# Performance work log

Measured on AMD Instinct MI355X. Metric: run time of the kernel, lower is better.

## Reference

```python
import jax, jax.numpy as jnp
import numpy as np

B, M, KM, D, H, L = 8, 2048, 1024, 256, 4, 2
HD = D // H

def _sp(x):
    return jnp.logaddexp(x, 0.0)  # softplus

def _rot_half(x):
    s = x.shape
    x = x.reshape(s[:-1] + (s[-1] // 2, 2))
    return jnp.stack((-x[..., 1], x[..., 0]), -1).reshape(s)

def _posenc(Wr, xy):
    # LearnableFourierPositionalEncoding(2, head_dim): rotary cos/sin embedding
    proj = xy @ Wr.T                                     # [N, HD//2]
    emb = jnp.stack((jnp.cos(proj), jnp.sin(proj)), 0)   # [2, N, HD//2]
    return jnp.repeat(emb, 2, axis=-1)                   # [2, N, HD]

def _heads(t):
    return t.reshape(t.shape[0], H, HD).transpose(1, 0, 2)  # [H, N, HD]

def _unheads(t):
    return t.transpose(1, 0, 2).reshape(t.shape[1], D)

def _ffn(x, m, W1, b1, g, be, W2, b2):
    h = jnp.concatenate([x, m], -1) @ W1.T + b1
    mu = h.mean(-1, keepdims=True)
    v = ((h - mu) ** 2).mean(-1, keepdims=True)
    h = (h - mu) * jax.lax.rsqrt(v + 1e-5) * g + be
    return x + jax.nn.gelu(h, approximate=False) @ W2.T + b2

def _self_block(x, enc, Wqkv, bqkv, Wo, bo, W1, b1, g, be, W2, b2):
    N = x.shape[0]
    qkv = (x @ Wqkv.T + bqkv).reshape(N, H, HD, 3).transpose(1, 0, 2, 3)  # [H,N,HD,3]
    q, k, v = qkv[..., 0], qkv[..., 1], qkv[..., 2]
    q = q * enc[0] + _rot_half(q) * enc[1]
    k = k * enc[0] + _rot_half(k) * enc[1]
    attn = jax.nn.softmax(jnp.einsum('hid,hjd->hij', q, k) / jnp.sqrt(jnp.float32(HD)), -1)
    msg = _unheads(jnp.einsum('hij,hjd->hid', attn, v)) @ Wo.T + bo
    return _ffn(x, msg, W1, b1, g, be, W2, b2)

def _cross_block(x0, x1, Wqk, bqk, Wv, bv, Wo, bo, W1, b1, g, be, W2, b2):
    sc = HD ** -0.25
    qk0 = _heads(x0 @ Wqk.T + bqk) * sc
    qk1 = _heads(x1 @ Wqk.T + bqk) * sc
    v0 = _heads(x0 @ Wv.T + bv)
    v1 = _heads(x1 @ Wv.T + bv)
    sim = jnp.einsum('hid,hjd->hij', qk0, qk1)
    m0 = _unheads(jnp.einsum('hij,hjd->hid', jax.nn.softmax(sim, -1), v1)) @ Wo.T + bo
    m1 = _unheads(jnp.einsum('hij,hid->hjd', jax.nn.softmax(sim, -2), v0)) @ Wo.T + bo
    return _ffn(x0, m0, W1, b1, g, be, W2, b2), _ffn(x1, m1, W1, b1, g, be, W2, b2)

def _forward(features_a, features_b, matches, kpts_a, kpts_b, lam, beta, Wr,
             pW1, pb1, pW2, pb2,
             sWqkv, sbqkv, sWo, sbo, sW1, sb1, sg, sbe, sW2, sb2,
             cWqk, cbqk, cWv, cbv, cWo, cbo, cW1, cb1, cg, cbe, cW2, cb2):
    lam_r = _sp(lam) + 1e-6
    beta_r = _sp(beta)
    eye = jnp.eye(KM, dtype=jnp.float32)

    def per_sample(fa, fb, match, ka, kb):
        ia, ib = match[:, 0], match[:, 1]
        f_i = fb[ib] - fa[ia]                                   # [KM, D]
        xy0, xy1 = ka[ia, :2], kb[ib, :2]                       # [KM, 2]
        d2 = jnp.sum((xy0[:, None, :] - xy0[None, :, :]) ** 2, -1)
        Kmat = jnp.exp(-beta_r * d2)                            # Gaussian RKHS kernel
        Lc = jnp.linalg.cholesky(Kmat + lam_r * eye)
        C = jax.scipy.linalg.cho_solve((Lc, True), f_i)         # [KM, D]
        f_glob = (Kmat / (Kmat.sum(-1, keepdims=True) + 1e-6)) @ C
        enc0, enc1 = _posenc(Wr, xy0), _posenc(Wr, xy1)
        d0, d1 = f_i, f_glob
        for l in range(L):
            d0 = _self_block(d0, enc0, sWqkv[l], sbqkv[l], sWo[l], sbo[l], sW1[l], sb1[l], sg[l], sbe[l], sW2[l], sb2[l])
            d1 = _self_block(d1, enc1, sWqkv[l], sbqkv[l], sWo[l], sbo[l], sW1[l], sb1[l], sg[l], sbe[l], sW2[l], sb2[l])
            d0, d1 = _cross_block(d0, d1, cWqk[l], cbqk[l], cWv[l], cbv[l], cWo[l], cbo[l], cW1[l], cb1[l], cg[l], cbe[l], cW2[l], cb2[l])
        h = jax.nn.relu(d0 @ pW1.T + pb1)
        return jax.nn.sigmoid(h @ pW2.T + pb2)[:, 0]            # [KM]

    return jax.vmap(per_sample)(features_a, features_b, matches, kpts_a, kpts_b)

def setup_inputs() -> dict:
    key = jax.random.key(0)
    ks = iter(jax.random.split(key, 64))
    def n(shape, s=0.02):
        return jax.random.normal(next(ks), shape, jnp.float32) * s
    return {
        'features_a': n((B, M, D), 1.0),
        'features_b': n((B, M, D), 1.0),
        'matches': jax.random.randint(next(ks), (B, KM, 2), 0, M),
        'kpts_a': jax.random.uniform(next(ks), (B, M, 2), jnp.float32) * 32.0,
        'kpts_b': jax.random.uniform(next(ks), (B, M, 2), jnp.float32) * 32.0,
        'lam': jnp.float32(0.1),
        'beta': jnp.float32(1.0),
        'Wr': n((HD // 2, 2), 1.0),
        'pW1': n((64, D)), 'pb1': jnp.zeros((64,), jnp.float32),
        'pW2': n((1, 64)), 'pb2': jnp.zeros((1,), jnp.float32),
        'sWqkv': n((L, 3 * D, D)), 'sbqkv': jnp.zeros((L, 3 * D), jnp.float32),
        'sWo': n((L, D, D)), 'sbo': jnp.zeros((L, D), jnp.float32),
        'sW1': n((L, 2 * D, 2 * D)), 'sb1': jnp.zeros((L, 2 * D), jnp.float32),
        'sg': jnp.ones((L, 2 * D), jnp.float32), 'sbe': jnp.zeros((L, 2 * D), jnp.float32),
        'sW2': n((L, D, 2 * D)), 'sb2': jnp.zeros((L, D), jnp.float32),
        'cWqk': n((L, D, D)), 'cbqk': jnp.zeros((L, D), jnp.float32),
        'cWv': n((L, D, D)), 'cbv': jnp.zeros((L, D), jnp.float32),
        'cWo': n((L, D, D)), 'cbo': jnp.zeros((L, D), jnp.float32),
        'cW1': n((L, 2 * D, 2 * D)), 'cb1': jnp.zeros((L, 2 * D), jnp.float32),
        'cg': jnp.ones((L, 2 * D), jnp.float32), 'cbe': jnp.zeros((L, 2 * D), jnp.float32),
        'cW2': n((L, D, 2 * D)), 'cb2': jnp.zeros((L, D), jnp.float32),
    }

def reference(features_a, features_b, matches, kpts_a, kpts_b, lam, beta, Wr,
              pW1, pb1, pW2, pb2,
              sWqkv, sbqkv, sWo, sbo, sW1, sb1, sg, sbe, sW2, sb2,
              cWqk, cbqk, cWv, cbv, cWo, cbo, cW1, cb1, cg, cbe, cW2, cb2):
    return _forward(features_a, features_b, matches, kpts_a, kpts_b, lam, beta, Wr,
                    pW1, pb1, pW2, pb2,
                    sWqkv, sbqkv, sWo, sbo, sW1, sb1, sg, sbe, sW2, sb2,
                    cWqk, cbqk, cWv, cbv, cWo, cbo, cW1, cb1, cg, cbe, cW2, cb2)
```

## Files before the change

kernel.cpp:

```cpp
#include <hip/hip_runtime.h>
#include <math.h>

#define BB 8
#define MM 2048
#define KM 1024
#define DD 256
#define HH 4
#define HD 64
#define NLAYER 2
#define BN (BB*KM)
#define N2 (2*BN)
#define CG_ITERS 5

#define SWZ(r,c) (((r)<<6) + ((((c)>>3) ^ ((r)&7))<<3) + ((c)&7))

typedef __bf16 bf16;
typedef __bf16 bf16x8 __attribute__((ext_vector_type(8)));
typedef __bf16 bf16x4 __attribute__((ext_vector_type(4)));
typedef __bf16 bf16x2 __attribute__((ext_vector_type(2)));
typedef _Float16 fp16;
typedef _Float16 fp16x8 __attribute__((ext_vector_type(8)));
typedef short  short4v __attribute__((ext_vector_type(4)));
typedef float  floatx4 __attribute__((ext_vector_type(4)));
#define MFMA16(a,b,c)  __builtin_amdgcn_mfma_f32_16x16x32_bf16(a,b,c,0,0,0)
#define MFMA16H(a,b,c) __builtin_amdgcn_mfma_f32_16x16x32_f16(a,b,c,0,0,0)

#if defined(__HIP_DEVICE_COMPILE__)
  #if __has_builtin(__builtin_amdgcn_mfma_f32_16x16x16bf16_1k)
    #define MFMA1K(a,b,c) __builtin_amdgcn_mfma_f32_16x16x16bf16_1k(a,b,c,0,0,0)
  #else
    #error "device pass lacks mfma_f32_16x16x16bf16_1k"
  #endif
#else
  #define MFMA1K(a,b,c) (c)
#endif

__device__ __forceinline__ float softplusf(float x) {
  return fmaxf(x, 0.f) + log1pf(expf(-fabsf(x)));
}

__device__ __forceinline__ float wred(float x) {
  x += __shfl_xor(x, 1);  x += __shfl_xor(x, 2);  x += __shfl_xor(x, 4);
  x += __shfl_xor(x, 8);  x += __shfl_xor(x, 16); x += __shfl_xor(x, 32);
  return x;
}

__device__ __forceinline__ short4v pack4(float a, float b, float c, float d) {
  bf16x4 v = {(bf16)a,(bf16)b,(bf16)c,(bf16)d};
  short4v s;
  __builtin_memcpy(&s, &v, 8);
  return s;
}

__device__ __forceinline__ void stage8(bf16* dst, const float* src) {
  float4 a = *(const float4*)src;
  float4 b = *(const float4*)(src + 4);
  bf16x8 v = { (bf16)a.x,(bf16)a.y,(bf16)a.z,(bf16)a.w,
               (bf16)b.x,(bf16)b.y,(bf16)b.z,(bf16)b.w };
  *(bf16x8*)dst = v;
}
__device__ __forceinline__ void stage8(bf16* dst, const bf16* src) {
  *(uint4*)dst = *(const uint4*)src;
}

template<typename T> struct Raw8;
template<> struct Raw8<float> {
  float4 a, b;
  __device__ __forceinline__ void load(const float* s) {
    a = *(const float4*)s; b = *(const float4*)(s + 4);
  }
  __device__ __forceinline__ void store(fp16* d) const {
    fp16x8 v = { (fp16)a.x,(fp16)a.y,(fp16)a.z,(fp16)a.w,
                 (fp16)b.x,(fp16)b.y,(fp16)b.z,(fp16)b.w };
    *(fp16x8*)d = v;
  }
  __device__ __forceinline__ void storeb(bf16* d) const {
    bf16x8 v = { (bf16)a.x,(bf16)a.y,(bf16)a.z,(bf16)a.w,
                 (bf16)b.x,(bf16)b.y,(bf16)b.z,(bf16)b.w };
    *(bf16x8*)d = v;
  }
};
template<> struct Raw8<fp16> {
  uint4 u;
  __device__ __forceinline__ void load(const fp16* s) { u = *(const uint4*)s; }
  __device__ __forceinline__ void store(fp16* d) const { *(uint4*)d = u; }
};

__global__ __launch_bounds__(256) void gather_kernel(
    const float* __restrict__ fa, const float* __restrict__ fb,
    const int* __restrict__ matches, const float* __restrict__ ka,
    const float* __restrict__ kb, float* __restrict__ F,
    float* __restrict__ Fd,
    float* __restrict__ xy0, float* __restrict__ xy1)
{
  int si = blockIdx.x;
  int s  = si >> 10;
  int t  = threadIdx.x;
  int ia = matches[(size_t)si*2+0];
  int ib = matches[(size_t)si*2+1];
  float v = fb[((size_t)s*MM + ib)*DD + t] - fa[((size_t)s*MM + ia)*DD + t];
  F[(size_t)si*DD + t]  = v;
  Fd[(size_t)si*DD + t] = v;
  if (t == 0) {
    xy0[(size_t)si*2+0] = ka[((size_t)s*MM + ia)*2+0];
    xy0[(size_t)si*2+1] = ka[((size_t)s*MM + ia)*2+1];
    xy1[(size_t)si*2+0] = kb[((size_t)s*MM + ib)*2+0];
    xy1[(size_t)si*2+1] = kb[((size_t)s*MM + ib)*2+1];
  }
}

__global__ __launch_bounds__(256) void posenc_kernel(
    const float* __restrict__ xy, const float* __restrict__ Wr,
    float* __restrict__ enc)
{
  int t = threadIdx.x;
  int si = blockIdx.x*4 + (t >> 6);
  int s = si >> 10, i = si & 1023;
  int d = t & 63; int p = d >> 1;
  float x = xy[(size_t)si*2], y = xy[(size_t)si*2+1];
  float pr = Wr[p*2]*x + Wr[p*2+1]*y;
  enc[(((size_t)s*2+0)*KM + i)*HD + d] = cosf(pr);
  enc[(((size_t)s*2+1)*KM + i)*HD + d] = sinf(pr);
}

__global__ __launch_bounds__(256) void kmat_kernel(
    const float* __restrict__ xy0, const float* __restrict__ beta_ptr,
    fp16* __restrict__ Km, float* __restrict__ rowsum)
{
  __shared__ float redw[4];
  int si = blockIdx.x; int s = si >> 10;
  int t = threadIdx.x;
  int lane = t & 63, w = t >> 6;
  float beta_l2 = softplusf(beta_ptr[0]) * 1.442695040888963f;
  float xi = xy0[(size_t)si*2], yi = xy0[(size_t)si*2+1];
  const float* xys = xy0 + (size_t)s*KM*2;
  float sum = 0.f;
  for (int jj = 0; jj < 4; ++jj) {
    int j = jj*256 + t;
    float dx = xi - xys[j*2], dy = yi - xys[j*2+1];
    float v = exp2f(-beta_l2*(dx*dx + dy*dy));
    Km[(size_t)si*KM + j] = (fp16)v;
    sum += v;
  }
  sum = wred(sum);
  if (lane == 0) redw[w] = sum;
  __syncthreads();
  if (t == 0)
    rowsum[si] = ((redw[0]+redw[1]) + (redw[2]+redw[3])) + 1e-6f;
}

template<int NT, int WPERM, int DUALW,
         typename TA1, typename TA2, typename TW, typename TO>
__global__ __launch_bounds__(256) void mm_kernel(
    const TA1* __restrict__ A1, const TA2* __restrict__ A2, int K1, int K,
    const TW* __restrict__ W, const float* __restrict__ bias,
    const TW* __restrict__ Wb, const float* __restrict__ biasb,
    TO* __restrict__ C, int O, float scale, float scaleb,
    const float* __restrict__ resid)
{
  __shared__ __align__(16) bf16 Al[128*72];
  __shared__ __align__(16) bf16 Wl[NT*72];
  constexpr int MB = (NT == 128) ? 4 : 2;
  constexpr int WP = NT/32;
  int tid = threadIdx.x;
  int row0 = blockIdx.x*128, col0 = blockIdx.y*NT;
  int lane = tid & 63, w = tid >> 6;
  int wr = (NT == 128) ? (w>>1)*64 : w*32;
  int wc = (NT == 128) ? (w&1)*64 : 0;
  int lm = lane & 15, lq = lane >> 4;
  int srow = tid >> 3, sc8 = (tid & 7)*8;

  const TA1* aptr1[4]; const TA2* aptr2[4];
#pragma unroll
  for (int p = 0; p < 4; ++p) {
    int row = p*32 + srow;
    aptr1[p] = A1 + (size_t)(row0+row)*K1 + sc8;
    aptr2[p] = A2 + (size_t)(row0+row)*(K-K1) + sc8;
  }
  const TW* wptr[WP];
#pragma unroll
  for (int p = 0; p < WP; ++p) {
    int wg = col0 + p*32 + srow;
    const TW* wsrc; int wrow;
    if (DUALW && wg >= 256) { wsrc = Wb; wrow = wg - 256; }
    else { wsrc = W; wrow = WPERM ? ((wg & 255)*3 + (wg >> 8)) : wg; }
    wptr[p] = wsrc + (size_t)wrow*K + sc8;
  }

  floatx4 acc[MB][4];
#pragma unroll
  for (int mb = 0; mb < MB; ++mb)
#pragma unroll
    for (int nb = 0; nb < 4; ++nb) acc[mb][nb] = (floatx4){0.f,0.f,0.f,0.f};
  for (int k0 = 0; k0 < K; k0 += 64) {
    bool use1 = (k0 < K1);
#pragma unroll
    for (int p = 0; p < 4; ++p) {
      bf16* d = &Al[(p*32+srow)*72 + sc8];
      if (use1) stage8(d, aptr1[p] + k0);
      else      stage8(d, aptr2[p] + (k0 - K1));
    }
#pragma unroll
    for (int p = 0; p < WP; ++p)
      stage8(&Wl[(p*32+srow)*72 + sc8], wptr[p] + k0);
    __syncthreads();
    bf16x8 af[MB][2], bfr[4][2];
#pragma unroll
    for (int mb = 0; mb < MB; ++mb) {
      af[mb][0] = *(bf16x8*)&Al[(wr + mb*16 + lm)*72 + lq*8];
      af[mb][1] = *(bf16x8*)&Al[(wr + mb*16 + lm)*72 + 32 + lq*8];
    }
#pragma unroll
    for (int nb = 0; nb < 4; ++nb) {
      bfr[nb][0] = *(bf16x8*)&Wl[(wc + nb*16 + lm)*72 + lq*8];
      bfr[nb][1] = *(bf16x8*)&Wl[(wc + nb*16 + lm)*72 + 32 + lq*8];
    }
    __builtin_amdgcn_s_setprio(1);
#pragma unroll
    for (int mb = 0; mb < MB; ++mb)
#pragma unroll
      for (int nb = 0; nb < 4; ++nb) {
        acc[mb][nb] = MFMA16(af[mb][0], bfr[nb][0], acc[mb][nb]);
        acc[mb][nb] = MFMA16(af[mb][1], bfr[nb][1], acc[mb][nb]);
      }
    __builtin_amdgcn_s_setprio(0);
    __syncthreads();
  }
#pragma unroll
  for (int mb = 0; mb < MB; ++mb) {
#pragma unroll
    for (int nb = 0; nb < 4; ++nb) {
#pragma unroll
      for (int r = 0; r < 4; ++r) {
        int grow = row0 + wr + mb*16 + lq*4 + r;
        int gcol = col0 + wc + nb*16 + lm;
        float v = acc[mb][nb][r];
        float bv = 0.f, scl = scale;
        if (DUALW && gcol >= 256) {
          if (biasb) bv = biasb[gcol - 256];
          scl = scaleb;
        } else if (bias) {
          bv = bias[WPERM ? ((gcol & 255)*3 + (gcol >> 8)) : gcol];
        }
        v = (v + bv) * scl;
        if (resid) v += resid[(size_t)grow*O + gcol];
        C[(size_t)grow*O + gcol] = (TO)v;
      }
    }
  }
}

template<typename TO>
__global__ __launch_bounds__(256) void mm64d_kernel(
    const bf16* __restrict__ A, int K, const float* __restrict__ W,
    const float* __restrict__ bias, TO* __restrict__ C, int O,
    const float* __restrict__ resid)
{
  __shared__ __align__(16) bf16 Al[2][64*72];
  __shared__ __align__(16) bf16 Wl[2][64*72];
  int tid = threadIdx.x;
  int row0 = blockIdx.x*64, col0 = blockIdx.y*64;
  int lane = tid & 63, w = tid >> 6;
  int wr = (w>>1)*32, wc = (w&1)*32;
  int lm = lane & 15, lq = lane >> 4;
  int sr0 = tid >> 3, c8 = (tid & 7)*8;
  int sr1 = sr0 + 32;
  const bf16*  a0ptr = A + (size_t)(row0+sr0)*K + c8;
  const bf16*  a1ptr = A + (size_t)(row0+sr1)*K + c8;
  const float* w0ptr = W + (size_t)(col0+sr0)*K + c8;
  const float* w1ptr = W + (size_t)(col0+sr1)*K + c8;

  floatx4 acc[2][2];
#pragma unroll
  for (int mb = 0; mb < 2; ++mb)
#pragma unroll
    for (int nb = 0; nb < 2; ++nb) acc[mb][nb] = (floatx4){0.f,0.f,0.f,0.f};

  uint4 ra0 = *(const uint4*)a0ptr;
  uint4 ra1 = *(const uint4*)a1ptr;
  Raw8<float> rw0, rw1;
  rw0.load(w0ptr); rw1.load(w1ptr);
  *(uint4*)&Al[0][sr0*72 + c8] = ra0;
  *(uint4*)&Al[0][sr1*72 + c8] = ra1;
  rw0.storeb(&Wl[0][sr0*72 + c8]);
  rw1.storeb(&Wl[0][sr1*72 + c8]);
  __syncthreads();

  for (int k0 = 0; k0 < K; k0 += 64) {
    int cur = (k0 >> 6) & 1;
    bool pre = (k0 + 64 < K);
    if (pre) {
      ra0 = *(const uint4*)(a0ptr + k0 + 64);
      ra1 = *(const uint4*)(a1ptr + k0 + 64);
      rw0.load(w0ptr + k0 + 64);
      rw1.load(w1ptr + k0 + 64);
    }
    bf16x8 af0[2], af1[2], b0[2], b1[2];
#pragma unroll
    for (int mb = 0; mb < 2; ++mb) {
      af0[mb] = *(bf16x8*)&Al[cur][(wr + mb*16 + lm)*72 + lq*8];
      af1[mb] = *(bf16x8*)&Al[cur][(wr + mb*16 + lm)*72 + 32 + lq*8];
    }
#pragma unroll
    for (int nb = 0; nb < 2; ++nb) {
      b0[nb] = *(bf16x8*)&Wl[cur][(wc + nb*16 + lm)*72 + lq*8];
      b1[nb] = *(bf16x8*)&Wl[cur][(wc + nb*16 + lm)*72 + 32 + lq*8];
    }
    __builtin_amdgcn_s_setprio(1);
#pragma unroll
    for (int mb = 0; mb < 2; ++mb)
#pragma unroll
      for (int nb = 0; nb < 2; ++nb) {
        acc[mb][nb] = MFMA16(af0[mb], b0[nb], acc[mb][nb]);
        acc[mb][nb] = MFMA16(af1[mb], b1[nb], acc[mb][nb]);
      }
    __builtin_amdgcn_s_setprio(0);
    if (pre) {
      *(uint4*)&Al[cur^1][sr0*72 + c8] = ra0;
      *(uint4*)&Al[cur^1][sr1*72 + c8] = ra1;
      rw0.storeb(&Wl[cur^1][sr0*72 + c8]);
      rw1.storeb(&Wl[cur^1][sr1*72 + c8]);
    }
    __syncthreads();
  }
#pragma unroll
  for (int mb = 0; mb < 2; ++mb) {
#pragma unroll
    for (int nb = 0; nb < 2; ++nb) {
#pragma unroll
      for (int r = 0; r < 4; ++r) {
        int grow = row0 + wr + mb*16 + lq*4 + r;
        int gcol = col0 + wc + nb*16 + lm;
        float v = acc[mb][nb][r] + bias[gcol];
        if (resid) v += resid[(size_t)grow*O + gcol];
        C[(size_t)grow*O + gcol] = (TO)v;
      }
    }
  }
}

template<typename TA, typename TW, typename TO>
__global__ __launch_bounds__(256) void mv64_kernel(
    const TA* __restrict__ A, int K, const TW* __restrict__ W,
    TO* __restrict__ C, int O,
    const float* __restrict__ resid, const float* __restrict__ lam_ptr,
    const float* __restrict__ rowdiv,
    long zsA, long zsW, long zsC, long zsR)
{
  __shared__ __align__(16) fp16 Al[2][64*72];
  __shared__ __align__(16) fp16 Wl[2][64*72];
  int tid = threadIdx.x;
  int z = blockIdx.z;
  const TA* Az = A + (size_t)z*zsA;
  const TW* Wz = W + (size_t)z*zsW;
  TO* Cz = C + (size_t)z*zsC;
  const float* Rz = resid ? (resid + (size_t)z*zsR) : (const float*)0;
  int row0 = blockIdx.x*64, col0 = blockIdx.y*64;
  int lane = tid & 63, w = tid >> 6;
  int wr = (w>>1)*32, wc = (w&1)*32;
  int lm = lane & 15, lq = lane >> 4;
  int sr0 = tid >> 3, c8 = (tid & 7)*8;
  int sr1 = sr0 + 32;
  floatx4 acc[2][2];
#pragma unroll
  for (int mb = 0; mb < 2; ++mb)
#pragma unroll
    for (int nb = 0; nb < 2; ++nb) acc[mb][nb] = (floatx4){0.f,0.f,0.f,0.f};

  Raw8<TA> a0p, a1p; Raw8<TW> w0p, w1p;
  a0p.load(&Az[(size_t)(row0+sr0)*K + c8]);
  a1p.load(&Az[(size_t)(row0+sr1)*K + c8]);
  w0p.load(&Wz[(size_t)(col0+sr0)*K + c8]);
  w1p.load(&Wz[(size_t)(col0+sr1)*K + c8]);
  a0p.store(&Al[0][sr0*72 + c8]); a1p.store(&Al[0][sr1*72 + c8]);
  w0p.store(&Wl[0][sr0*72 + c8]); w1p.store(&Wl[0][sr1*72 + c8]);
  __syncthreads();

  for (int k0 = 0; k0 < K; k0 += 64) {
    int cur = (k0 >> 6) & 1;
    bool pre = (k0 + 64 < K);
    if (pre) {
      a0p.load(&Az[(size_t)(row0+sr0)*K + k0+64 + c8]);
      a1p.load(&Az[(size_t)(row0+sr1)*K + k0+64 + c8]);
      w0p.load(&Wz[(size_t)(col0+sr0)*K + k0+64 + c8]);
      w1p.load(&Wz[(size_t)(col0+sr1)*K + k0+64 + c8]);
    }
    fp16x8 a0[2], a1[2], b0[2], b1[2];
#pragma unroll
    for (int mb = 0; mb < 2; ++mb) {
      a0[mb] = *(fp16x8*)&Al[cur][(wr + mb*16 + lm)*72 + lq*8];
      a1[mb] = *(fp16x8*)&Al[cur][(wr + mb*16 + lm)*72 + 32 + lq*8];
    }
#pragma unroll
    for (int nb = 0; nb < 2; ++nb) {
      b0[nb] = *(fp16x8*)&Wl[cur][(wc + nb*16 + lm)*72 + lq*8];
      b1[nb] = *(fp16x8*)&Wl[cur][(wc + nb*16 + lm)*72 + 32 + lq*8];
    }
    __builtin_amdgcn_s_setprio(1);
#pragma unroll
    for (int mb = 0; mb < 2; ++mb)
#pragma unroll
      for (int nb = 0; nb < 2; ++nb) {
        acc[mb][nb] = MFMA16H(a0[mb], b0[nb], acc[mb][nb]);
        acc[mb][nb] = MFMA16H(a1[mb], b1[nb], acc[mb][nb]);
      }
    __builtin_amdgcn_s_setprio(0);
    if (pre) {
      a0p.store(&Al[cur^1][sr0*72 + c8]); a1p.store(&Al[cur^1][sr1*72 + c8]);
      w0p.store(&Wl[cur^1][sr0*72 + c8]); w1p.store(&Wl[cur^1][sr1*72 + c8]);
    }
    __syncthreads();
  }
  float lamv = 1.f;
  if (lam_ptr) lamv = softplusf(lam_ptr[0]) + 1e-6f;
#pragma unroll
  for (int mb = 0; mb < 2; ++mb) {
#pragma unroll
    for (int nb = 0; nb < 2; ++nb) {
#pragma unroll
      for (int r = 0; r < 4; ++r) {
        int grow = row0 + wr + mb*16 + lq*4 + r;
        int gcol = col0 + wc + nb*16 + lm;
        float v = acc[mb][nb][r];
        if (rowdiv) v /= rowdiv[(size_t)z*KM + grow];
        if (Rz) v += lamv * Rz[(size_t)grow*O + gcol];
        Cz[(size_t)grow*O + gcol] = (TO)v;
      }
    }
  }
}

__global__ __launch_bounds__(256) void gemm_f32_kernel(
    const float* __restrict__ A, int K,
    const float* __restrict__ W, const float* __restrict__ bias,
    float* __restrict__ C, int O)
{
  __shared__ float As[32][68];
  __shared__ float Ws[32][68];
  int t = threadIdx.x;
  int row0 = blockIdx.x * 64;
  int col0 = blockIdx.y * 64;
  int ti = t & 15, tj = t >> 4;
  float acc[4][4] = {};
  for (int k0 = 0; k0 < K; k0 += 32) {
#pragma unroll
    for (int p = 0; p < 2; ++p) {
      int idx = p*256 + t;
      int ar = idx >> 3, af = (idx & 7)*4;
      float4 av = *(const float4*)&A[(size_t)(row0+ar)*K + k0 + af];
      As[af+0][ar] = av.x; As[af+1][ar] = av.y;
      As[af+2][ar] = av.z; As[af+3][ar] = av.w;
      float4 wv = *(const float4*)&W[(size_t)(col0+ar)*K + k0 + af];
      Ws[af+0][ar] = wv.x; Ws[af+1][ar] = wv.y;
      Ws[af+2][ar] = wv.z; Ws[af+3][ar] = wv.w;
    }
    __syncthreads();
#pragma unroll
    for (int kk = 0; kk < 32; ++kk) {
      float4 a4 = *(float4*)&As[kk][ti*4];
      float4 b4 = *(float4*)&Ws[kk][tj*4];
      float a[4] = {a4.x, a4.y, a4.z, a4.w};
      float b[4] = {b4.x, b4.y, b4.z, b4.w};
#pragma unroll
      for (int x = 0; x < 4; ++x)
#pragma unroll
        for (int y = 0; y < 4; ++y) acc[x][y] += a[x]*b[y];
    }
    __syncthreads();
  }
#pragma unroll
  for (int x = 0; x < 4; ++x) {
    int r = row0 + ti*4 + x;
#pragma unroll
    for (int y = 0; y < 4; ++y) {
      int c = col0 + tj*4 + y;
      float v = fmaxf(acc[x][y] + bias[c], 0.f);
      C[(size_t)r*O + c] = v;
    }
  }
}

__global__ __launch_bounds__(256) void tinit_kernel(
    const float* __restrict__ F, float* __restrict__ PT, float* __restrict__ RT,
    float* __restrict__ XT)
{
  __shared__ float Ls[64][68];
  int t = threadIdx.x;
  int k0 = blockIdx.x*64, n0 = blockIdx.y*64, z = blockIdx.z;
#pragma unroll
  for (int p = 0; p < 4; ++p) {
    int idx = p*256 + t;
    int kr = idx >> 4, c4 = (idx & 15)*4;
    *(float4*)&Ls[kr][c4] = *(const float4*)&F[((size_t)z*KM + k0+kr)*DD + n0 + c4];
  }
  __syncthreads();
#pragma unroll
  for (int p = 0; p < 4; ++p) {
    int idx = p*256 + t;
    int nl = idx >> 4, k4 = (idx & 15)*4;
    float4 v = { Ls[k4+0][nl], Ls[k4+1][nl], Ls[k4+2][nl], Ls[k4+3][nl] };
    size_t o = ((size_t)z*DD + n0+nl)*KM + k0 + k4;
    *(float4*)&PT[o] = v;
    *(float4*)&RT[o] = v;
    float4 zr = {0.f,0.f,0.f,0.f};
    *(float4*)&XT[o] = zr;
  }
}

__global__ __launch_bounds__(256) void cg_update_kernel(
    float* __restrict__ XT, float* __restrict__ RT,
    float* __restrict__ PT, const float* __restrict__ APT)
{
  __shared__ float redw[12];
  int row = blockIdx.x;
  int t = threadIdx.x;
  int lane = t & 63, w = t >> 6;
  size_t base = (size_t)row*KM + (size_t)t*4;
  float4 p4 = *(float4*)&PT[base];
  float4 a4 = *(const float4*)&APT[base];
  float4 r4 = *(float4*)&RT[base];
  float4 x4 = *(float4*)&XT[base];
  float prr  = (r4.x*r4.x + r4.y*r4.y) + (r4.z*r4.z + r4.w*r4.w);
  float ppap = (p4.x*a4.x + p4.y*a4.y) + (p4.z*a4.z + p4.w*a4.w);
  prr = wred(prr); ppap = wred(ppap);
  if (lane == 0) { redw[w] = prr; redw[4+w] = ppap; }
  __syncthreads();
  float rr  = (redw[0]+redw[1]) + (redw[2]+redw[3]);
  float pap = (redw[4]+redw[5]) + (redw[6]+redw[7]);
  float alpha = (pap > 1e-30f) ? rr/pap : 0.f;
  x4.x += alpha*p4.x; x4.y += alpha*p4.y; x4.z += alpha*p4.z; x4.w += alpha*p4.w;
  r4.x -= alpha*a4.x; r4.y -= alpha*a4.y; r4.z -= alpha*a4.z; r4.w -= alpha*a4.w;
  *(float4*)&XT[base] = x4;
  *(float4*)&RT[base] = r4;
  float s = (r4.x*r4.x + r4.y*r4.y) + (r4.z*r4.z + r4.w*r4.w);
  s = wred(s);
  if (lane == 0) redw[8+w] = s;
  __syncthreads();
  float rrnew = (redw[8]+redw[9]) + (redw[10]+redw[11]);
  float beta = (rr > 1e-30f) ? rrnew/rr : 0.f;
  p4.x = r4.x + beta*p4.x; p4.y = r4.y + beta*p4.y;
  p4.z = r4.z + beta*p4.z; p4.w = r4.w + beta*p4.w;
  *(float4*)&PT[base] = p4;
}

__global__ __launch_bounds__(256) void rope_split_kernel(
    const bf16* __restrict__ qkv, const float* __restrict__ enc0,
    const float* __restrict__ enc1, bf16* __restrict__ Qo,
    bf16* __restrict__ Ko)
{
  int t = threadIdx.x;
  int r = blockIdx.x*2 + (t >> 7);
  int c = (t & 127)*2;
  int ts = r >> 10, i = r & 1023;
  int d = c & 63;
  const float* enc = (ts < BB) ? enc0 : enc1;
  int s = (ts < BB) ? ts : ts - BB;
  const float* eb = enc + (((size_t)s*2)*KM + i)*HD;
  float2 cs = *(const float2*)&eb[d];
  float2 sn = *(const float2*)&eb[(size_t)KM*HD + d];
  size_t base = (size_t)r*768;
  bf16x2 qv = *(const bf16x2*)&qkv[base + c];
  bf16x2 kv = *(const bf16x2*)&qkv[base + 256 + c];
  float q0 = (float)qv[0], q1 = (float)qv[1];
  float k0 = (float)kv[0], k1 = (float)kv[1];
  float oq0 = q0*cs.x - q1*sn.x, oq1 = q1*cs.y + q0*sn.y;
  float ok0 = k0*cs.x - k1*sn.x, ok1 = k1*cs.y + k0*sn.y;
  size_t o = (size_t)r*DD + c;
  bf16x2 qo = {(bf16)(0.1803368801f*oq0), (bf16)(0.1803368801f*oq1)};
  bf16x2 ko = {(bf16)ok0, (bf16)ok1};
  *(bf16x2*)&Qo[o] = qo;
  *(bf16x2*)&Ko[o] = ko;
}

__global__ __launch_bounds__(256) void vt_kernel(
    const bf16* __restrict__ Vin, int vstride, bf16* __restrict__ VT)
{
  __shared__ __align__(16) bf16 Ls[64*72];
  int tid = threadIdx.x;
  int zh = blockIdx.x;
  int ts = zh >> 2, h = zh & 3;
  int k0 = blockIdx.y * 64;
#pragma unroll
  for (int p = 0; p < 2; ++p) {
    int idx = p*256 + tid;
    int kr = idx >> 3, c8 = (idx & 7)*8;
    *(uint4*)&Ls[kr*72 + c8] =
      *(const uint4*)&Vin[((size_t)ts*KM + k0 + kr)*vstride + h*HD + c8];
  }
  __syncthreads();
#pragma unroll
  for (int p = 0; p < 2; ++p) {
    int idx = p*256 + tid;
    int dr = idx >> 3, k8 = (idx & 7)*8;
    bf16 tmp[8] __attribute__((aligned(16)));
#pragma unroll
    for (int j = 0; j < 8; ++j) tmp[j] = Ls[(k8+j)*72 + dr];
    *(uint4*)&VT[((size_t)zh*HD + dr)*KM + k0 + k8] = *(uint4*)tmp;
  }
}

__device__ __forceinline__ void mha_body(
    const bf16* __restrict__ Qg, const bf16* __restrict__ Kg,
    const bf16* __restrict__ VTg, bf16* __restrict__ Og,
    size_t qkbase, size_t obase, size_t vbase, int qkstride,
    int q0, int tid, bf16* Qs, bf16* Ks, bf16* Vt)
{
  int lane = tid & 63, w = tid >> 6;
  int lm = lane & 15, lq = lane >> 4;
  int r0 = tid >> 3, c8 = (tid & 7)*8;
  int r1 = r0 + 32;
  *(uint4*)&Qs[SWZ(r0,c8)] = *(const uint4*)&Qg[qkbase + (size_t)(q0+r0)*qkstride + c8];
  *(uint4*)&Qs[SWZ(r1,c8)] = *(const uint4*)&Qg[qkbase + (size_t)(q0+r1)*qkstride + c8];
  __syncthreads();
  bf16x8 qa0 = *(bf16x8*)&Qs[SWZ(w*16 + lm, lq*8)];
  bf16x8 qa1 = *(bf16x8*)&Qs[SWZ(w*16 + lm, 32 + lq*8)];
  short4v ones4;
  { bf16x4 o1 = {(bf16)1.f,(bf16)1.f,(bf16)1.f,(bf16)1.f};
    __builtin_memcpy(&ones4, &o1, 8); }
  float m_ = 0.f;
  floatx4 lacc = (floatx4){0.f,0.f,0.f,0.f};
  floatx4 oacc[4];
#pragma unroll
  for (int db = 0; db < 4; ++db) oacc[db] = (floatx4){0.f,0.f,0.f,0.f};

  for (int kt = 0; kt < KM; kt += 64) {
    __syncthreads();
    *(uint4*)&Ks[SWZ(r0,c8)] = *(const uint4*)&Kg[qkbase + (size_t)(kt+r0)*qkstride + c8];
    *(uint4*)&Ks[SWZ(r1,c8)] = *(const uint4*)&Kg[qkbase + (size_t)(kt+r1)*qkstride + c8];
    *(uint4*)&Vt[SWZ(r0,c8)] = *(const uint4*)&VTg[vbase + (size_t)r0*KM + kt + c8];
    *(uint4*)&Vt[SWZ(r1,c8)] = *(const uint4*)&VTg[vbase + (size_t)r1*KM + kt + c8];
    __syncthreads();
    floatx4 st[4];
    float negm = -m_;
    __builtin_amdgcn_s_setprio(1);
#pragma unroll
    for (int kb = 0; kb < 4; ++kb) {
      bf16x8 a0 = *(bf16x8*)&Ks[SWZ(kb*16 + lm, lq*8)];
      bf16x8 a1 = *(bf16x8*)&Ks[SWZ(kb*16 + lm, 32 + lq*8)];
      floatx4 acc = (floatx4){negm, negm, negm, negm};
      acc = MFMA16(a0, qa0, acc);
      acc = MFMA16(a1, qa1, acc);
      st[kb] = acc;
    }
    __builtin_amdgcn_s_setprio(0);
    float ma = fmaxf(fmaxf(st[0][0], st[0][1]), st[0][2]);
    float mb = fmaxf(fmaxf(st[0][3], st[1][0]), st[1][1]);
    float mc = fmaxf(fmaxf(st[1][2], st[1][3]), st[2][0]);
    float md = fmaxf(fmaxf(st[2][1], st[2][2]), st[2][3]);
    float me = fmaxf(fmaxf(st[3][0], st[3][1]), st[3][2]);
    float mf = fmaxf(fmaxf(ma, mb), st[3][3]);
    float mg = fmaxf(fmaxf(mc, md), me);
    float mx = fmaxf(mf, mg);
    if (!__all(mx <= 8.f)) {
      float wmx = fmaxf(mx, __shfl_xor(mx, 16));
      wmx = fmaxf(wmx, __shfl_xor(wmx, 32));
      float delta = fmaxf(wmx, 0.f);
      float al = exp2f(-delta);
      m_ += delta;
      lacc[0] *= al; lacc[1] *= al; lacc[2] *= al; lacc[3] *= al;
#pragma unroll
      for (int db = 0; db < 4; ++db) {
        oacc[db][0] *= al; oacc[db][1] *= al;
        oacc[db][2] *= al; oacc[db][3] *= al;
      }
#pragma unroll
      for (int kb = 0; kb < 4; ++kb) {
        st[kb][0] -= delta; st[kb][1] -= delta;
        st[kb][2] -= delta; st[kb][3] -= delta;
      }
    }
    __builtin_amdgcn_s_setprio(1);
#pragma unroll
    for (int kb = 0; kb < 4; ++kb) {
      float p0 = exp2f(st[kb][0]);
      float p1 = exp2f(st[kb][1]);
      float p2 = exp2f(st[kb][2]);
      float p3 = exp2f(st[kb][3]);
      short4v pb = pack4(p0, p1, p2, p3);
      lacc = MFMA1K(ones4, pb, lacc);
#pragma unroll
      for (int db = 0; db < 4; ++db) {
        short4v va = *(const short4v*)&Vt[SWZ(db*16 + lm, kb*16 + lq*4)];
        oacc[db] = MFMA1K(va, pb, oacc[db]);
      }
    }
    __builtin_amdgcn_s_setprio(0);
  }
  float inv = 1.f / lacc[0];
  int q = q0 + w*16 + lm;
#pragma unroll
  for (int db = 0; db < 4; ++db) {
    bf16x4 o4 = { (bf16)(oacc[db][0]*inv), (bf16)(oacc[db][1]*inv),
                  (bf16)(oacc[db][2]*inv), (bf16)(oacc[db][3]*inv) };
    *(bf16x4*)&Og[obase + (size_t)q*DD + db*16 + lq*4] = o4;
  }
}

__global__ __launch_bounds__(256) void mha_kernel(
    const bf16* __restrict__ Qg, const bf16* __restrict__ Kg,
    const bf16* __restrict__ VTg, bf16* __restrict__ Og)
{
  __shared__ __align__(16) bf16 Qs[64*64];
  __shared__ __align__(16) bf16 Ks[64*64];
  __shared__ __align__(16) bf16 Vt[64*64];
  int zh = blockIdx.x;
  int z = zh >> 2, h = zh & 3;
  size_t base = ((size_t)z*KM)*DD + (size_t)h*HD;
  size_t vbase = (size_t)zh*HD*KM;
  mha_body(Qg, Kg, VTg, Og, base, base, vbase, DD,
           blockIdx.y*64, threadIdx.x, Qs, Ks, Vt);
}

__global__ __launch_bounds__(256) void mha_cross_kernel(
    const bf16* __restrict__ QKV2, const bf16* __restrict__ VT2,
    bf16* __restrict__ ATTO2)
{
  __shared__ __align__(16) bf16 Qs[64*64];
  __shared__ __align__(16) bf16 Ks[64*64];
  __shared__ __align__(16) bf16 Vt[64*64];
  int dir = blockIdx.z;
  const bf16* Qg  = QKV2 + (dir ? (size_t)BN*512 : 0);
  const bf16* Kg  = QKV2 + (dir ? 0 : (size_t)BN*512);
  const bf16* VTg = VT2  + (dir ? 0 : (size_t)32*HD*KM);
  bf16*       Og  = ATTO2 + (dir ? (size_t)BN*DD : 0);
  int zh = blockIdx.x;
  int z = zh >> 2, h = zh & 3;
  size_t qkbase = ((size_t)z*KM)*512 + (size_t)h*HD;
  size_t obase  = ((size_t)z*KM)*DD  + (size_t)h*HD;
  size_t vbase  = (size_t)zh*HD*KM;
  mha_body(Qg, Kg, VTg, Og, qkbase, obase, vbase, 512,
           blockIdx.y*64, threadIdx.x, Qs, Ks, Vt);
}

__global__ __launch_bounds__(256) void ln_gelu_kernel(
    bf16* __restrict__ Hb, const float* __restrict__ g,
    const float* __restrict__ be)
{
  int t = threadIdx.x;
  int lane = t & 63, w = t >> 6;
  size_t r = (size_t)blockIdx.x*4 + w;
  bf16* rowp = Hb + r*512 + lane*8;
  bf16x8 hv = *(bf16x8*)rowp;
  float x[8];
#pragma unroll
  for (int j = 0; j < 8; ++j) x[j] = (float)hv[j];
  float s = ((x[0]+x[1]) + (x[2]+x[3])) + ((x[4]+x[5]) + (x[6]+x[7]));
  s = wred(s);
  float mu = s * (1.f/512.f);
  float v = 0.f;
#pragma unroll
  for (int j = 0; j < 8; ++j) { float d = x[j] - mu; v += d*d; }
  v = wred(v);
  float rstd = rsqrtf(v*(1.f/512.f) + 1e-5f);
  float4 g0 = *(const float4*)&g[lane*8];
  float4 g1 = *(const float4*)&g[lane*8 + 4];
  float4 b0 = *(const float4*)&be[lane*8];
  float4 b1 = *(const float4*)&be[lane*8 + 4];
  float gv[8] = {g0.x,g0.y,g0.z,g0.w,g1.x,g1.y,g1.z,g1.w};
  float bv[8] = {b0.x,b0.y,b0.z,b0.w,b1.x,b1.y,b1.z,b1.w};
  bf16x8 ov;
#pragma unroll
  for (int j = 0; j < 8; ++j) {
    float h = (x[j] - mu)*rstd*gv[j] + bv[j];
    h = 0.5f*h*(1.f + erff(h*0.70710678118f));
    ov[j] = (bf16)h;
  }
  *(bf16x8*)rowp = ov;
}

__global__ __launch_bounds__(256) void head2_kernel(
    const float* __restrict__ Hb, const float* __restrict__ w,
    const float* __restrict__ b, float* __restrict__ out)
{
  int r = blockIdx.x*256 + threadIdx.x;
  float acc = b[0];
#pragma unroll
  for (int k = 0; k < 64; ++k) acc += Hb[(size_t)r*64 + k]*w[k];
  out[r] = 1.f/(1.f + expf(-acc));
}

extern "C" void kernel_launch(void* const* d_in, const int* in_sizes, int n_in,
                              void* d_out, int out_size, void* d_ws, size_t ws_size,
                              hipStream_t stream)
{
  (void)in_sizes; (void)n_in; (void)out_size; (void)ws_size;
  const float* fa      = (const float*)d_in[0];
  const float* fb      = (const float*)d_in[1];
  const int*   matches = (const int*)d_in[2];
  const float* ka      = (const float*)d_in[3];
  const float* kb      = (const float*)d_in[4];
  const float* lam     = (const float*)d_in[5];
  const float* beta    = (const float*)d_in[6];
  const float* Wr      = (const float*)d_in[7];
  const float* pW1     = (const float*)d_in[8];
  const float* pb1     = (const float*)d_in[9];
  const float* pW2     = (const float*)d_in[10];
  const float* pb2     = (const float*)d_in[11];
  const float* sWqkv   = (const float*)d_in[12];
  const float* sbqkv   = (const float*)d_in[13];
  const float* sWo     = (const float*)d_in[14];
  const float* sbo     = (const float*)d_in[15];
  const float* sW1     = (const float*)d_in[16];
  const float* sb1     = (const float*)d_in[17];
  const float* sg      = (const float*)d_in[18];
  const float* sbe     = (const float*)d_in[19];
  const float* sW2     = (const float*)d_in[20];
  const float* sb2     = (const float*)d_in[21];
  const float* cWqk    = (const float*)d_in[22];
  const float* cbqk    = (const float*)d_in[23];
  const float* cWv     = (const float*)d_in[24];
  const float* cbv     = (const float*)d_in[25];
  const float* cWo     = (const float*)d_in[26];
  const float* cbo     = (const float*)d_in[27];
  const float* cW1     = (const float*)d_in[28];
  const float* cb1     = (const float*)d_in[29];
  const float* cgw     = (const float*)d_in[30];
  const float* cbe     = (const float*)d_in[31];
  const float* cW2     = (const float*)d_in[32];
  const float* cb2     = (const float*)d_in[33];

  char* wsb = (char*)d_ws;
  float* DCAT = (float*)wsb;
  float* ENC0 = (float*)(wsb + 16777216);
  float* ENC1 = (float*)(wsb + 20971520);
  float* XY0  = (float*)(wsb + 25165824);
  float* XY1  = (float*)(wsb + 25231360);
  float* ROWS = (float*)(wsb + 25296896);
  char*  POOL = wsb + 25354240;
  const size_t SLOT = 8388608;
  fp16*  KMATH = (fp16*)POOL;
  float* FBUF  = (float*)(POOL + 2*SLOT);
  float* PT    = (float*)(POOL + 3*SLOT);
  float* RT    = (float*)(POOL + 4*SLOT);
  float* XT    = (float*)(POOL + 5*SLOT);
  float* APT   = (float*)(POOL + 6*SLOT);
  bf16*  QKV   = (bf16*)POOL;
  bf16*  QR    = (bf16*)(POOL + 3*SLOT);
  bf16*  KR    = (bf16*)(POOL + 4*SLOT);
  bf16*  VTG   = (bf16*)(POOL + 8*SLOT);
  bf16*  ATTO  = (bf16*)POOL;
  bf16*  MSG   = (bf16*)(POOL + 1*SLOT);
  bf16*  H1    = (bf16*)(POOL + 6*SLOT);
  bf16*  QKV2  = (bf16*)POOL;
  bf16*  ATTO2 = (bf16*)(POOL + 2*SLOT);
  bf16*  MSG2  = (bf16*)(POOL + 3*SLOT);
  bf16*  VT2   = (bf16*)(POOL + 4*SLOT);
  bf16*  H1C   = H1;
  float* HBUF  = (float*)POOL;

  const float scq = 0.42466090f;

  gather_kernel<<<BN, 256, 0, stream>>>(fa, fb, matches, ka, kb, FBUF, DCAT, XY0, XY1);
  posenc_kernel<<<BN/4, 256, 0, stream>>>(XY0, Wr, ENC0);
  posenc_kernel<<<BN/4, 256, 0, stream>>>(XY1, Wr, ENC1);
  kmat_kernel<<<BN, 256, 0, stream>>>(XY0, beta, KMATH, ROWS);

  tinit_kernel<<<dim3(16,4,BB), 256, 0, stream>>>(FBUF, PT, RT, XT);
  for (int it = 0; it < CG_ITERS; ++it) {
    mv64_kernel<float,fp16,float><<<dim3(4,16,BB), 256, 0, stream>>>(
        PT, 1024, KMATH, APT, 1024, PT, lam, (const float*)0,
        262144, 1048576, 262144, 262144);
    cg_update_kernel<<<2048, 256, 0, stream>>>(XT, RT, PT, APT);
  }

  mv64_kernel<fp16,float,float><<<dim3(16,4,BB), 256, 0, stream>>>(
      KMATH, 1024, XT, DCAT + (size_t)BN*DD, 256,
      (const float*)0, (const float*)0, ROWS,
      1048576, 262144, 262144, 0);

  for (int l = 0; l < NLAYER; ++l) {
    mm_kernel<128,1,0,float,float,float,bf16><<<dim3(128,6,1), 256, 0, stream>>>(
        DCAT, (const float*)0, 256, 256, sWqkv + (size_t)l*768*256, sbqkv + l*768,
        (const float*)0, (const float*)0, QKV, 768, 1.f, 1.f, (const float*)0);
    rope_split_kernel<<<8192, 256, 0, stream>>>(QKV, ENC0, ENC1, QR, KR);
    vt_kernel<<<dim3(64,16), 256, 0, stream>>>(QKV + 512, 768, VTG);
    mha_kernel<<<dim3(64,16), 256, 0, stream>>>(QR, KR, VTG, ATTO);
    mm64d_kernel<bf16><<<dim3(256,4,1), 256, 0, stream>>>(
        ATTO, 256, sWo + (size_t)l*256*256, sbo + l*256, MSG, 256,
        (const float*)0);
    mm_kernel<128,0,0,float,bf16,float,bf16><<<dim3(128,4,1), 256, 0, stream>>>(
        DCAT, MSG, 256, 512, sW1 + (size_t)l*512*512, sb1 + l*512,
        (const float*)0, (const float*)0, H1, 512, 1.f, 1.f, (const float*)0);
    ln_gelu_kernel<<<N2/4, 256, 0, stream>>>(H1, sg + l*512, sbe + l*512);
    mm64d_kernel<float><<<dim3(256,4,1), 256, 0, stream>>>(
        H1, 512, sW2 + (size_t)l*256*512, sb2 + l*256, DCAT, 256, DCAT);
    mm_kernel<128,0,1,float,float,float,bf16><<<dim3(128,4,1), 256, 0, stream>>>(
        DCAT, (const float*)0, 256, 256, cWqk + (size_t)l*256*256, cbqk + l*256,
        cWv + (size_t)l*256*256, cbv + l*256, QKV2, 512, scq, 1.f,
        (const float*)0);
    vt_kernel<<<dim3(64,16), 256, 0, stream>>>(QKV2 + 256, 512, VT2);
    mha_cross_kernel<<<dim3(32,16,2), 256, 0, stream>>>(QKV2, VT2, ATTO2);
    mm64d_kernel<bf16><<<dim3(256,4,1), 256, 0, stream>>>(
        ATTO2, 256, cWo + (size_t)l*256*256, cbo + l*256, MSG2, 256,
        (const float*)0);
    mm_kernel<128,0,0,float,bf16,float,bf16><<<dim3(128,4,1), 256, 0, stream>>>(
        DCAT, MSG2, 256, 512, cW1 + (size_t)l*512*512, cb1 + l*512,
        (const float*)0, (const float*)0, H1C, 512, 1.f, 1.f, (const float*)0);
    ln_gelu_kernel<<<N2/4, 256, 0, stream>>>(H1C, cgw + l*512, cbe + l*512);
    mm64d_kernel<float><<<dim3(256,4,1), 256, 0, stream>>>(
        H1C, 512, cW2 + (size_t)l*256*512, cb2 + l*256, DCAT, 256, DCAT);
  }

  gemm_f32_kernel<<<dim3(128,1), 256, 0, stream>>>(DCAT, 256, pW1, pb1, HBUF, 64);
  head2_kernel<<<32, 256, 0, stream>>>(HBUF, pW2, pb2, (float*)d_out);
}
```

Measured before the change: 928.7 us.

## Replace 128-row GEMM with double-buffered 64x64 tile kernel

Replaces the 128xNT single-buffered GEMM used for the QKV, FFN-W1 and cross QK/V projections with a 64x64-tile kernel. It double-buffers the shared memory tiles and prefetches the next K slice into registers while the MFMAs run, so global loads overlap with compute. The smaller tiles launch many more blocks to improve occupancy and load balance. In exchange each block reuses its loaded operands less, so global and L2 traffic for A and W rises.

```diff
diff --git a/kernel.cpp b/kernel.cpp
--- a/kernel.cpp
+++ b/kernel.cpp
@@ -52,17 +52,6 @@
   return s;
 }
 
-__device__ __forceinline__ void stage8(bf16* dst, const float* src) {
-  float4 a = *(const float4*)src;
-  float4 b = *(const float4*)(src + 4);
-  bf16x8 v = { (bf16)a.x,(bf16)a.y,(bf16)a.z,(bf16)a.w,
-               (bf16)b.x,(bf16)b.y,(bf16)b.z,(bf16)b.w };
-  *(bf16x8*)dst = v;
-}
-__device__ __forceinline__ void stage8(bf16* dst, const bf16* src) {
-  *(uint4*)dst = *(const uint4*)src;
-}
-
 template<typename T> struct Raw8;
 template<> struct Raw8<float> {
   float4 a, b;
@@ -84,6 +73,11 @@
   uint4 u;
   __device__ __forceinline__ void load(const fp16* s) { u = *(const uint4*)s; }
   __device__ __forceinline__ void store(fp16* d) const { *(uint4*)d = u; }
+};
+template<> struct Raw8<bf16> {
+  uint4 u;
+  __device__ __forceinline__ void load(const bf16* s) { u = *(const uint4*)s; }
+  __device__ __forceinline__ void storeb(bf16* d) const { *(uint4*)d = u; }
 };
 
 __global__ __launch_bounds__(256) void gather_kernel(
@@ -149,87 +143,110 @@
     rowsum[si] = ((redw[0]+redw[1]) + (redw[2]+redw[3])) + 1e-6f;
 }
 
-template<int NT, int WPERM, int DUALW,
-         typename TA1, typename TA2, typename TW, typename TO>
-__global__ __launch_bounds__(256) void mm_kernel(
+template<int WPERM, int DUALW, typename TA1, typename TA2, typename TO>
+__global__ __launch_bounds__(256) void mm64g_kernel(
     const TA1* __restrict__ A1, const TA2* __restrict__ A2, int K1, int K,
-    const TW* __restrict__ W, const float* __restrict__ bias,
-    const TW* __restrict__ Wb, const float* __restrict__ biasb,
+    const float* __restrict__ W, const float* __restrict__ bias,
+    const float* __restrict__ Wb, const float* __restrict__ biasb,
     TO* __restrict__ C, int O, float scale, float scaleb,
     const float* __restrict__ resid)
 {
-  __shared__ __align__(16) bf16 Al[128*72];
-  __shared__ __align__(16) bf16 Wl[NT*72];
-  constexpr int MB = (NT == 128) ? 4 : 2;
-  constexpr int WP = NT/32;
+  __shared__ __align__(16) bf16 Al[2][64*72];
+  __shared__ __align__(16) bf16 Wl[2][64*72];
   int tid = threadIdx.x;
-  int row0 = blockIdx.x*128, col0 = blockIdx.y*NT;
+  int row0 = blockIdx.x*64, col0 = blockIdx.y*64;
   int lane = tid & 63, w = tid >> 6;
-  int wr = (NT == 128) ? (w>>1)*64 : w*32;
-  int wc = (NT == 128) ? (w&1)*64 : 0;
+  int wr = (w>>1)*32, wc = (w&1)*32;
   int lm = lane & 15, lq = lane >> 4;
-  int srow = tid >> 3, sc8 = (tid & 7)*8;
-
-  const TA1* aptr1[4]; const TA2* aptr2[4];
-#pragma unroll
-  for (int p = 0; p < 4; ++p) {
-    int row = p*32 + srow;
-    aptr1[p] = A1 + (size_t)(row0+row)*K1 + sc8;
-    aptr2[p] = A2 + (size_t)(row0+row)*(K-K1) + sc8;
-  }
-  const TW* wptr[WP];
-#pragma unroll
-  for (int p = 0; p < WP; ++p) {
-    int wg = col0 + p*32 + srow;
-    const TW* wsrc; int wrow;
-    if (DUALW && wg >= 256) { wsrc = Wb; wrow = wg - 256; }
-    else { wsrc = W; wrow = WPERM ? ((wg & 255)*3 + (wg >> 8)) : wg; }
-    wptr[p] = wsrc + (size_t)wrow*K + sc8;
-  }
-
-  floatx4 acc[MB][4];
-#pragma unroll
-  for (int mb = 0; mb < MB; ++mb)
-#pragma unroll
-    for (int nb = 0; nb < 4; ++nb) acc[mb][nb] = (floatx4){0.f,0.f,0.f,0.f};
-  for (int k0 = 0; k0 < K; k0 += 64) {
-    bool use1 = (k0 < K1);
-#pragma unroll
-    for (int p = 0; p < 4; ++p) {
-      bf16* d = &Al[(p*32+srow)*72 + sc8];
-      if (use1) stage8(d, aptr1[p] + k0);
-      else      stage8(d, aptr2[p] + (k0 - K1));
-    }
-#pragma unroll
-    for (int p = 0; p < WP; ++p)
-      stage8(&Wl[(p*32+srow)*72 + sc8], wptr[p] + k0);
+  int sr0 = tid >> 3, c8 = (tid & 7)*8;
+  int sr1 = sr0 + 32;
+  int K2 = K - K1;
+
+  const TA1* a1p0 = A1 + (size_t)(row0+sr0)*K1 + c8;
+  const TA1* a1p1 = A1 + (size_t)(row0+sr1)*K1 + c8;
+  const TA2* a2p0 = A2 + (size_t)(row0+sr0)*K2 + c8;
+  const TA2* a2p1 = A2 + (size_t)(row0+sr1)*K2 + c8;
+  const float* wp0; const float* wp1;
+  {
+    int wg0 = col0 + sr0, wg1 = col0 + sr1;
+    const float* ws0; int wrow0;
+    if (DUALW && wg0 >= 256) { ws0 = Wb; wrow0 = wg0 - 256; }
+    else { ws0 = W; wrow0 = WPERM ? ((wg0 & 255)*3 + (wg0 >> 8)) : wg0; }
+    const float* ws1; int wrow1;
+    if (DUALW && wg1 >= 256) { ws1 = Wb; wrow1 = wg1 - 256; }
+    else { ws1 = W; wrow1 = WPERM ? ((wg1 & 255)*3 + (wg1 >> 8)) : wg1; }
+    wp0 = ws0 + (size_t)wrow0*K + c8;
+    wp1 = ws1 + (size_t)wrow1*K + c8;
+  }
+
+  floatx4 acc[2][2];
+#pragma unroll
+  for (int mb = 0; mb < 2; ++mb)
+#pragma unroll
+    for (int nb = 0; nb < 2; ++nb) acc[mb][nb] = (floatx4){0.f,0.f,0.f,0.f};
+
+  Raw8<TA1> ra1_0, ra1_1; Raw8<TA2> ra2_0, ra2_1;
+  Raw8<float> rw_0, rw_1;
+  {
+    bool u0 = (0 < K1);
+    if (u0) { ra1_0.load(a1p0); ra1_1.load(a1p1); }
+    else    { ra2_0.load(a2p0); ra2_1.load(a2p1); }
+    rw_0.load(wp0); rw_1.load(wp1);
+    if (u0) { ra1_0.storeb(&Al[0][sr0*72 + c8]); ra1_1.storeb(&Al[0][sr1*72 + c8]); }
+    else    { ra2_0.storeb(&Al[0][sr0*72 + c8]); ra2_1.storeb(&Al[0][sr1*72 + c8]); }
+    rw_0.storeb(&Wl[0][sr0*72 + c8]);
+    rw_1.storeb(&Wl[0][sr1*72 + c8]);
     __syncthreads();
-    bf16x8 af[MB][2], bfr[4][2];
-#pragma unroll
-    for (int mb = 0; mb < MB; ++mb) {
-      af[mb][0] = *(bf16x8*)&Al[(wr + mb*16 + lm)*72 + lq*8];
-      af[mb][1] = *(bf16x8*)&Al[(wr + mb*16 + lm)*72 + 32 + lq*8];
-    }
-#pragma unroll
-    for (int nb = 0; nb < 4; ++nb) {
-      bfr[nb][0] = *(bf16x8*)&Wl[(wc + nb*16 + lm)*72 + lq*8];
-      bfr[nb][1] = *(bf16x8*)&Wl[(wc + nb*16 + lm)*72 + 32 + lq*8];
+  }
+
+  int nst = K >> 6;
+  for (int j = 0; j < nst; ++j) {
+    int cur = j & 1;
+    bool pre = (j + 1 < nst);
+    bool nUse1 = (((j+1) << 6) < K1);
+    if (pre) {
+      int k1n = (j+1) << 6;
+      if (nUse1) { ra1_0.load(a1p0 + k1n); ra1_1.load(a1p1 + k1n); }
+      else       { ra2_0.load(a2p0 + (k1n - K1)); ra2_1.load(a2p1 + (k1n - K1)); }
+      rw_0.load(wp0 + k1n); rw_1.load(wp1 + k1n);
+    }
+    bf16x8 af0[2], af1[2], b0[2], b1[2];
+#pragma unroll
+    for (int mb = 0; mb < 2; ++mb) {
+      af0[mb] = *(bf16x8*)&Al[cur][(wr + mb*16 + lm)*72 + lq*8];
+      af1[mb] = *(bf16x8*)&Al[cur][(wr + mb*16 + lm)*72 + 32 + lq*8];
+    }
+#pragma unroll
+    for (int nb = 0; nb < 2; ++nb) {
+      b0[nb] = *(bf16x8*)&Wl[cur][(wc + nb*16 + lm)*72 + lq*8];
+      b1[nb] = *(bf16x8*)&Wl[cur][(wc + nb*16 + lm)*72 + 32 + lq*8];
     }
     __builtin_amdgcn_s_setprio(1);
 #pragma unroll
-    for (int mb = 0; mb < MB; ++mb)
-#pragma unroll
-      for (int nb = 0; nb < 4; ++nb) {
-        acc[mb][nb] = MFMA16(af[mb][0], bfr[nb][0], acc[mb][nb]);
-        acc[mb][nb] = MFMA16(af[mb][1], bfr[nb][1], acc[mb][nb]);
+    for (int mb = 0; mb < 2; ++mb)
+#pragma unroll
+      for (int nb = 0; nb < 2; ++nb) {
+        acc[mb][nb] = MFMA16(af0[mb], b0[nb], acc[mb][nb]);
+        acc[mb][nb] = MFMA16(af1[mb], b1[nb], acc[mb][nb]);
       }
     __builtin_amdgcn_s_setprio(0);
+    if (pre) {
+      if (nUse1) {
+        ra1_0.storeb(&Al[cur^1][sr0*72 + c8]);
+        ra1_1.storeb(&Al[cur^1][sr1*72 + c8]);
+      } else {
+        ra2_0.storeb(&Al[cur^1][sr0*72 + c8]);
+        ra2_1.storeb(&Al[cur^1][sr1*72 + c8]);
+      }
+      rw_0.storeb(&Wl[cur^1][sr0*72 + c8]);
+      rw_1.storeb(&Wl[cur^1][sr1*72 + c8]);
+    }
     __syncthreads();
   }
 #pragma unroll
-  for (int mb = 0; mb < MB; ++mb) {
-#pragma unroll
-    for (int nb = 0; nb < 4; ++nb) {
+  for (int mb = 0; mb < 2; ++mb) {
+#pragma unroll
+    for (int nb = 0; nb < 2; ++nb) {
 #pragma unroll
       for (int r = 0; r < 4; ++r) {
         int grow = row0 + wr + mb*16 + lq*4 + r;
@@ -869,8 +886,8 @@
       1048576, 262144, 262144, 0);
 
   for (int l = 0; l < NLAYER; ++l) {
-    mm_kernel<128,1,0,float,float,float,bf16><<<dim3(128,6,1), 256, 0, stream>>>(
-        DCAT, (const float*)0, 256, 256, sWqkv + (size_t)l*768*256, sbqkv + l*768,
+    mm64g_kernel<1,0,float,bf16,bf16><<<dim3(256,12,1), 256, 0, stream>>>(
+        DCAT, (const bf16*)0, 256, 256, sWqkv + (size_t)l*768*256, sbqkv + l*768,
         (const float*)0, (const float*)0, QKV, 768, 1.f, 1.f, (const float*)0);
     rope_split_kernel<<<8192, 256, 0, stream>>>(QKV, ENC0, ENC1, QR, KR);
     vt_kernel<<<dim3(64,16), 256, 0, stream>>>(QKV + 512, 768, VTG);
@@ -878,14 +895,14 @@
     mm64d_kernel<bf16><<<dim3(256,4,1), 256, 0, stream>>>(
         ATTO, 256, sWo + (size_t)l*256*256, sbo + l*256, MSG, 256,
         (const float*)0);
-    mm_kernel<128,0,0,float,bf16,float,bf16><<<dim3(128,4,1), 256, 0, stream>>>(
+    mm64g_kernel<0,0,float,bf16,bf16><<<dim3(256,8,1), 256, 0, stream>>>(
         DCAT, MSG, 256, 512, sW1 + (size_t)l*512*512, sb1 + l*512,
         (const float*)0, (const float*)0, H1, 512, 1.f, 1.f, (const float*)0);
     ln_gelu_kernel<<<N2/4, 256, 0, stream>>>(H1, sg + l*512, sbe + l*512);
     mm64d_kernel<float><<<dim3(256,4,1), 256, 0, stream>>>(
         H1, 512, sW2 + (size_t)l*256*512, sb2 + l*256, DCAT, 256, DCAT);
-    mm_kernel<128,0,1,float,float,float,bf16><<<dim3(128,4,1), 256, 0, stream>>>(
-        DCAT, (const float*)0, 256, 256, cWqk + (size_t)l*256*256, cbqk + l*256,
+    mm64g_kernel<0,1,float,bf16,bf16><<<dim3(256,8,1), 256, 0, stream>>>(
+        DCAT, (const bf16*)0, 256, 256, cWqk + (size_t)l*256*256, cbqk + l*256,
         cWv + (size_t)l*256*256, cbv + l*256, QKV2, 512, scq, 1.f,
         (const float*)0);
     vt_kernel<<<dim3(64,16), 256, 0, stream>>>(QKV2 + 256, 512, VT2);
@@ -893,7 +910,7 @@
     mm64d_kernel<bf16><<<dim3(256,4,1), 256, 0, stream>>>(
         ATTO2, 256, cWo + (size_t)l*256*256, cbo + l*256, MSG2, 256,
         (const float*)0);
-    mm_kernel<128,0,0,float,bf16,float,bf16><<<dim3(128,4,1), 256, 0, stream>>>(
+    mm64g_kernel<0,0,float,bf16,bf16><<<dim3(256,8,1), 256, 0, stream>>>(
         DCAT, MSG2, 256, 512, cW1 + (size_t)l*512*512, cb1 + l*512,
         (const float*)0, (const float*)0, H1C, 512, 1.f, 1.f, (const float*)0);
     ln_gelu_kernel<<<N2/4, 256, 0, stream>>>(H1C, cgw + l*512, cbe + l*512);
```

New measurement: 901.0 us. 3.0% less time.
